# Optimization experiments

Hardware: AMD Instinct MI355X
Metric: run time of the kernel (lower is better)

Reference implementation:

```python
import jax, jax.numpy as jnp
import numpy as np

N, E = 50000, 800000
DIN, DH, H, DOUT = 128, 16, 8, 32  # hidden = H*DH = 128
NEG_SLOPE = 0.2


def setup_inputs() -> dict:
    key = jax.random.key(0)
    ks = jax.random.split(key, 10)
    g = lambda k, shape, fan: jax.random.normal(k, shape, jnp.float32) * (1.0 / np.sqrt(fan))
    return {
        "x": jax.random.normal(ks[0], (N, DIN), jnp.float32),
        "edge_index": jax.random.randint(ks[1], (2, E), 0, N, dtype=jnp.int64),
        # layer 1 (GATv2Conv(DIN, DH, heads=H), concat=True)
        "W1_src": g(ks[2], (DIN, H * DH), DIN),
        "W1_dst": g(ks[3], (DIN, H * DH), DIN),
        "b1_src": jnp.zeros((H * DH,), jnp.float32),
        "b1_dst": jnp.zeros((H * DH,), jnp.float32),
        "att1": g(ks[4], (H, DH), DH),
        "bias1": jnp.zeros((H * DH,), jnp.float32),
        # layer 2 (GATv2Conv(H*DH, DOUT, heads=1))
        "W2_src": g(ks[5], (H * DH, DOUT), H * DH),
        "W2_dst": g(ks[6], (H * DH, DOUT), H * DH),
        "b2_src": jnp.zeros((DOUT,), jnp.float32),
        "b2_dst": jnp.zeros((DOUT,), jnp.float32),
        "att2": g(ks[7], (1, DOUT), DOUT),
        "bias2": jnp.zeros((DOUT,), jnp.float32),
    }


def _gatv2(x, src, dst, Wsrc, Wdst, bsrc, bdst, att, bias):
    # GATv2 conv: e_ij = att . LeakyReLU(Wsrc x_j + Wdst x_i); softmax over j->i; out_i = sum alpha_ij * Wsrc x_j
    n = x.shape[0]
    h, c = att.shape
    xs = (x @ Wsrc + bsrc).reshape(n, h, c)  # source transform (messages)
    xd = (x @ Wdst + bdst).reshape(n, h, c)  # target transform
    msg = xs[src]  # [Etot, h, c]
    e = jax.nn.leaky_relu(msg + xd[dst], NEG_SLOPE)
    logits = jnp.einsum('ehc,hc->eh', e, att)  # [Etot, h]
    m = jax.lax.stop_gradient(jax.ops.segment_max(logits, dst, num_segments=n))
    ex = jnp.exp(logits - m[dst])
    denom = jax.ops.segment_sum(ex, dst, num_segments=n)
    alpha = ex / denom[dst]  # edge softmax per target node, per head
    out = jax.ops.segment_sum(alpha[..., None] * msg, dst, num_segments=n)
    return out.reshape(n, h * c) + bias  # concat=True


def reference(x, edge_index, W1_src, W1_dst, b1_src, b1_dst, att1, bias1,
              W2_src, W2_dst, b2_src, b2_dst, att2, bias2):
    n = x.shape[0]
    loop = jnp.arange(n, dtype=edge_index.dtype)  # add_self_loops=True (PyG default)
    src = jnp.concatenate([edge_index[0], loop])
    dst = jnp.concatenate([edge_index[1], loop])
    h1 = _gatv2(x, src, dst, W1_src, W1_dst, b1_src, b1_dst, att1, bias1)
    h1 = jax.nn.elu(h1)
    h2 = _gatv2(h1, src, dst, W2_src, W2_dst, b2_src, b2_dst, att2, bias2)  # heads=1 -> [N, DOUT]
    return jax.nn.log_softmax(h2, axis=1)
```

## Files before the change

### kernel.cpp

```cpp
#include <hip/hip_runtime.h>
#include <math.h>

#define NEG_SLOPE 0.2f

typedef __attribute__((ext_vector_type(8))) _Float16 h8v;
typedef __attribute__((ext_vector_type(2))) _Float16 h2v;
typedef __attribute__((ext_vector_type(4))) float float4v;

__device__ __forceinline__ h2v u2h(unsigned u) { return __builtin_bit_cast(h2v, u); }
__device__ __forceinline__ unsigned h2u(h2v h) { return __builtin_bit_cast(unsigned, h); }
__device__ __forceinline__ unsigned pk16(float a, float b) {
  h2v r; r.x = (_Float16)a; r.y = (_Float16)b;
  return __builtin_bit_cast(unsigned, r);
}
__device__ __forceinline__ unsigned short f16b(float f) {
  return __builtin_bit_cast(unsigned short, (_Float16)f);
}
__device__ __forceinline__ float fdot2(h2v a, h2v b, float c) {
#if __has_builtin(__builtin_amdgcn_fdot2)
  return __builtin_amdgcn_fdot2(a, b, c, false);
#else
  return fmaf((float)a.x, (float)b.x, fmaf((float)a.y, (float)b.y, c));
#endif
}

__device__ __forceinline__ int block_scan256(int v, int tid, int* ws) {
  const int lane = tid & 63, w = tid >> 6;
  int incl = v;
#pragma unroll
  for (int off = 1; off < 64; off <<= 1) {
    int t = __shfl_up(incl, off);
    if (lane >= off) incl += t;
  }
  if (lane == 63) ws[w] = incl;
  __syncthreads();
  if (tid == 0) {
    int s = 0;
#pragma unroll
    for (int i = 0; i < 4; i++) { int t = ws[i]; ws[4 + i] = s; s += t; }
  }
  __syncthreads();
  return incl - v + ws[4 + w];
}

__global__ __launch_bounds__(256) void pack_all(
    const float* __restrict__ W1s, const float* __restrict__ W1d,
    const float* __restrict__ W2s, const float* __restrict__ W2d,
    unsigned short* __restrict__ B1s, unsigned short* __restrict__ B1d,
    unsigned short* __restrict__ B2s, unsigned short* __restrict__ B2d) {
  int blk = blockIdx.x;
  const float* W; unsigned short* Bp; int C, base;
  if (blk < 8)       { W = W1s; Bp = B1s; C = 128; base = blk; }
  else if (blk < 16) { W = W1d; Bp = B1d; C = 128; base = blk - 8; }
  else if (blk < 18) { W = W2s; Bp = B2s; C = 32;  base = blk - 16; }
  else               { W = W2d; Bp = B2d; C = 32;  base = blk - 18; }
  int idx = base * 256 + threadIdx.x;
  int total = (C / 16) * 4 * 64;
  if (idx >= total) return;
  int lane = idx & 63;
  int kc = (idx >> 6) & 3;
  int t = idx >> 8;
  int n = t * 16 + (lane & 15);
  int k0 = kc * 32 + (lane >> 4) * 8;
  unsigned short* o = Bp + (size_t)idx * 8;
#pragma unroll
  for (int j = 0; j < 8; j++) o[j] = f16b(W[(size_t)(k0 + j) * C + n]);
}

template <int NT, int CVT>
__global__ __launch_bounds__(256) void mfma_xform2(
    const void* __restrict__ Xin,
    const unsigned short* __restrict__ BpS, const unsigned short* __restrict__ BpD,
    const float* __restrict__ bS, const float* __restrict__ bD,
    unsigned int* __restrict__ Ys, unsigned int* __restrict__ Yd, int M) {
  const int wave = threadIdx.x >> 6;
  const int lane = threadIdx.x & 63;
  const int row0 = blockIdx.x * 64 + wave * 16;
  const int m = lane & 15, q = lane >> 4;
  const int arow = min(row0 + m, M - 1);
  h8v a[4];
  if constexpr (CVT) {
    const float* xp = (const float*)Xin + (size_t)arow * 128 + q * 8;
#pragma unroll
    for (int kc = 0; kc < 4; kc++) {
      const float4 f0 = *(const float4*)(xp + kc * 32);
      const float4 f1 = *(const float4*)(xp + kc * 32 + 4);
      uint4 u;
      u.x = pk16(f0.x, f0.y); u.y = pk16(f0.z, f0.w);
      u.z = pk16(f1.x, f1.y); u.w = pk16(f1.z, f1.w);
      a[kc] = __builtin_bit_cast(h8v, u);
    }
  } else {
    const unsigned short* xp = (const unsigned short*)Xin + (size_t)arow * 128 + q * 8;
#pragma unroll
    for (int kc = 0; kc < 4; kc++) a[kc] = *(const h8v*)(xp + kc * 32);
  }
  float4v accS[NT], accD[NT];
#pragma unroll
  for (int t = 0; t < NT; t++) { accS[t] = (float4v)(0.f); accD[t] = (float4v)(0.f); }
#pragma unroll
  for (int kc = 0; kc < 4; kc++) {
#pragma unroll
    for (int t = 0; t < NT; t++) {
      h8v bs = *(const h8v*)(BpS + ((size_t)(t * 4 + kc) * 64 + lane) * 8);
      h8v bd = *(const h8v*)(BpD + ((size_t)(t * 4 + kc) * 64 + lane) * 8);
      accS[t] = __builtin_amdgcn_mfma_f32_16x16x32_f16(a[kc], bs, accS[t], 0, 0, 0);
      accD[t] = __builtin_amdgcn_mfma_f32_16x16x32_f16(a[kc], bd, accD[t], 0, 0, 0);
    }
  }
  const bool even = (m & 1) == 0;
#pragma unroll
  for (int t = 0; t < NT; t++) {
    const int col = t * 16 + m;
    const float bcS = bS[col], bcD = bD[col];
#pragma unroll
    for (int r = 0; r < 4; r++) {
      const int row = row0 + q * 4 + r;
      float vS = accS[t][r] + bcS;
      float vD = accD[t][r] + bcD;
      float pS = __shfl_xor(vS, 1);
      float pD = __shfl_xor(vD, 1);
      if (even && row < M) {
        size_t idx = (size_t)row * (NT * 8) + t * 8 + (m >> 1);
        Ys[idx] = pk16(vS, pS);
        Yd[idx] = pk16(vD, pD);
      }
    }
  }
}

__global__ __launch_bounds__(256) void bucket_hist(
    const int* __restrict__ ei, int* __restrict__ bhist, int N, int E, int NB) {
  __shared__ int cnt[256];
  const int tid = threadIdx.x;
  cnt[tid] = 0;
  __syncthreads();
  const int base = blockIdx.x * 4096;
  const int vn = min(4096, E - base);
#pragma unroll 4
  for (int j = 0; j < 16; j++) {
    int i = j * 256 + tid;
    if (i < vn) {
      int d = ei[E + base + i];
      d = min(max(d, 0), N - 1);
      atomicAdd(&cnt[d >> 8], 1);
    }
  }
  __syncthreads();
  if (tid < NB && cnt[tid]) atomicAdd(&bhist[tid], cnt[tid]);
}

__global__ __launch_bounds__(256) void bucket_scan(
    const int* __restrict__ bhist, int* __restrict__ bbase,
    int* __restrict__ bcur, int NB) {
  __shared__ int ws[8];
  const int tid = threadIdx.x;
  int v = (tid < NB) ? bhist[tid] : 0;
  int excl = block_scan256(v, tid, ws);
  if (tid <= NB) bbase[tid] = excl;
  if (tid < NB) bcur[tid] = excl;
}

__global__ __launch_bounds__(256) void bucket_sort(
    const int* __restrict__ ei, int* __restrict__ bcur,
    unsigned int* __restrict__ pairs, int N, int E, int NB) {
  __shared__ int cnt[256];
  __shared__ int offs[256];
  __shared__ int gbase[256];
  __shared__ int lcur[256];
  __shared__ int ws[8];
  __shared__ unsigned int packed_s[4096];
  __shared__ unsigned char bucket_of[4096];
  const int tid = threadIdx.x;
  cnt[tid] = 0;
  __syncthreads();
  const int base = blockIdx.x * 4096;
  const int vn = min(4096, E - base);
#pragma unroll 4
  for (int j = 0; j < 16; j++) {
    int i = j * 256 + tid;
    if (i < vn) {
      int d = ei[E + base + i];
      d = min(max(d, 0), N - 1);
      atomicAdd(&cnt[d >> 8], 1);
    }
  }
  __syncthreads();
  int excl = block_scan256(cnt[tid], tid, ws);
  offs[tid] = excl;
  lcur[tid] = excl;
  if (tid < NB && cnt[tid]) gbase[tid] = atomicAdd(&bcur[tid], cnt[tid]);
  __syncthreads();
#pragma unroll 4
  for (int j = 0; j < 16; j++) {
    int i = j * 256 + tid;
    if (i < vn) {
      int s = ei[base + i];
      int d = ei[E + base + i];
      s = min(max(s, 0), N - 1);
      d = min(max(d, 0), N - 1);
      int b = d >> 8;
      int slot = atomicAdd(&lcur[b], 1);
      packed_s[slot] = (unsigned)s | ((unsigned)(d & 255) << 16);
      bucket_of[slot] = (unsigned char)b;
    }
  }
  __syncthreads();
  for (int i = tid; i < vn; i += 256) {
    int b = bucket_of[i];
    pairs[gbase[b] + (i - offs[b])] = packed_s[i];
  }
}

__global__ __launch_bounds__(256) void csr_fine(
    const unsigned int* __restrict__ pairs, const int* __restrict__ bbase,
    int* __restrict__ row_ofs, int* __restrict__ src_sorted, int N, int E, int NB) {
  __shared__ int cnt[256];
  __shared__ int cursor[256];
  __shared__ int ws[8];
  const int tid = threadIdx.x;
  const int b = blockIdx.x;
  const int d0 = b << 8;
  const int nd = min(256, N - d0);
  const int pbase = bbase[b];
  const int pcnt = bbase[b + 1] - pbase;
  const int row_base = pbase + d0;
  cnt[tid] = (tid < nd) ? 1 : 0;
  __syncthreads();
  for (int i = tid; i < pcnt; i += 256) {
    unsigned p = pairs[pbase + i];
    atomicAdd(&cnt[(p >> 16) & 255], 1);
  }
  __syncthreads();
  int excl = block_scan256(cnt[tid], tid, ws);
  if (tid < nd) {
    row_ofs[d0 + tid] = row_base + excl;
    src_sorted[row_base + excl] = d0 + tid;
    cursor[tid] = excl + 1;
  }
  if (b == NB - 1 && tid == 0) row_ofs[N] = E + N;
  __syncthreads();
  for (int i = tid; i < pcnt; i += 256) {
    unsigned p = pairs[pbase + i];
    int dl = (p >> 16) & 255;
    int slot = atomicAdd(&cursor[dl], 1);
    src_sorted[row_base + slot] = (int)(p & 0xffffu);
  }
}

__global__ __launch_bounds__(256) void gat1_fused(
    const int* __restrict__ row_ofs, const int* __restrict__ src_sorted,
    const unsigned int* __restrict__ xsb, const unsigned int* __restrict__ xdb,
    const float* __restrict__ att, const float* __restrict__ bias,
    unsigned int* __restrict__ h1b, int N) {
  const int node = (int)((blockIdx.x * 256u + threadIdx.x) >> 6);
  const int lane = threadIdx.x & 63;
  const int l = lane & 15;
  const int g = lane >> 4;
  if (node >= N) return;
  h2v at2[4], xd[4];
  {
    const float4 a01 = *(const float4*)(att + 8 * l);
    const float4 a23 = *(const float4*)(att + 8 * l + 4);
    at2[0] = u2h(pk16(a01.x, a01.y)); at2[1] = u2h(pk16(a01.z, a01.w));
    at2[2] = u2h(pk16(a23.x, a23.y)); at2[3] = u2h(pk16(a23.z, a23.w));
    const uint4 xdp = *(const uint4*)(xdb + (unsigned)(node * 64 + 4 * l));
    xd[0] = u2h(xdp.x); xd[1] = u2h(xdp.y);
    xd[2] = u2h(xdp.z); xd[3] = u2h(xdp.w);
  }
  h2v ns; ns.x = (_Float16)NEG_SLOPE; ns.y = (_Float16)NEG_SLOPE;
  h2v acc[4];
#pragma unroll
  for (int i = 0; i < 4; i++) acc[i] = (h2v)((_Float16)0.f);
  float den = 0.f;
  const int b = row_ofs[node];
  const int cnt = row_ofs[node + 1] - b;
  for (int base = 0; base < cnt; base += 64) {
    const int rem = cnt - base;
    int sidx = (lane < rem) ? src_sorted[b + base + lane] : node;
    const int nIter = min(16, (rem + 3) >> 2);
    int s = __shfl(sidx, g);
    uint4 mp = *(const uint4*)(xsb + (unsigned)(s * 64 + 4 * l));
    for (int it = 0; it < nIter; it++) {
      const uint4 cur = mp;
      const bool v = (base + 4 * it + g) < cnt;
      if (it + 1 < nIter) {
        int sn = __shfl(sidx, 4 * (it + 1) + g);
        mp = *(const uint4*)(xsb + (unsigned)(sn * 64 + 4 * l));
      }
      const h2v m0 = u2h(cur.x), m1 = u2h(cur.y), m2 = u2h(cur.z), m3 = u2h(cur.w);
      h2v t0 = m0 + xd[0]; h2v r0 = __builtin_elementwise_max(t0, t0 * ns);
      h2v t1 = m1 + xd[1]; h2v r1 = __builtin_elementwise_max(t1, t1 * ns);
      h2v t2 = m2 + xd[2]; h2v r2 = __builtin_elementwise_max(t2, t2 * ns);
      h2v t3 = m3 + xd[3]; h2v r3 = __builtin_elementwise_max(t3, t3 * ns);
      float p = fdot2(r0, at2[0], 0.f);
      p = fdot2(r1, at2[1], p);
      p = fdot2(r2, at2[2], p);
      p = fdot2(r3, at2[3], p);
      p += __shfl_xor(p, 1);
      float ex = v ? __expf(p) : 0.f;
      den += ex;
      h2v exh; exh.x = exh.y = (_Float16)ex;
      acc[0] += m0 * exh;
      acc[1] += m1 * exh;
      acc[2] += m2 * exh;
      acc[3] += m3 * exh;
    }
  }
#pragma unroll
  for (int off = 16; off < 64; off <<= 1) {
#pragma unroll
    for (int i = 0; i < 4; i++) acc[i] += u2h(__shfl_xor(h2u(acc[i]), off));
    den += __shfl_xor(den, off);
  }
  if (lane < 16) {
    const float inv = 1.f / den;
    const float4 bc01 = *(const float4*)(bias + 8 * l);
    const float4 bc23 = *(const float4*)(bias + 8 * l + 4);
    float v0 = fmaf((float)acc[0].x, inv, bc01.x);
    float v1 = fmaf((float)acc[0].y, inv, bc01.y);
    float v2 = fmaf((float)acc[1].x, inv, bc01.z);
    float v3 = fmaf((float)acc[1].y, inv, bc01.w);
    float v4 = fmaf((float)acc[2].x, inv, bc23.x);
    float v5 = fmaf((float)acc[2].y, inv, bc23.y);
    float v6 = fmaf((float)acc[3].x, inv, bc23.z);
    float v7 = fmaf((float)acc[3].y, inv, bc23.w);
    v0 = v0 > 0.f ? v0 : __expf(v0) - 1.f;
    v1 = v1 > 0.f ? v1 : __expf(v1) - 1.f;
    v2 = v2 > 0.f ? v2 : __expf(v2) - 1.f;
    v3 = v3 > 0.f ? v3 : __expf(v3) - 1.f;
    v4 = v4 > 0.f ? v4 : __expf(v4) - 1.f;
    v5 = v5 > 0.f ? v5 : __expf(v5) - 1.f;
    v6 = v6 > 0.f ? v6 : __expf(v6) - 1.f;
    v7 = v7 > 0.f ? v7 : __expf(v7) - 1.f;
    uint4 o;
    o.x = pk16(v0, v1); o.y = pk16(v2, v3);
    o.z = pk16(v4, v5); o.w = pk16(v6, v7);
    *(uint4*)(h1b + (unsigned)(node * 64 + 4 * l)) = o;
  }
}

__global__ __launch_bounds__(256) void gat2_fused(
    const int* __restrict__ row_ofs, const int* __restrict__ src_sorted,
    const unsigned int* __restrict__ xsb, const unsigned int* __restrict__ xdb,
    const float* __restrict__ att, const float* __restrict__ bias,
    float* __restrict__ out, int N) {
  const int node = (int)((blockIdx.x * 256u + threadIdx.x) >> 6);
  const int lane = threadIdx.x & 63;
  const int l = lane & 3;
  const int g = lane >> 2;
  if (node >= N) return;
  h2v at2[4], xd[4];
  {
    const float4 a01 = *(const float4*)(att + 8 * l);
    const float4 a23 = *(const float4*)(att + 8 * l + 4);
    at2[0] = u2h(pk16(a01.x, a01.y)); at2[1] = u2h(pk16(a01.z, a01.w));
    at2[2] = u2h(pk16(a23.x, a23.y)); at2[3] = u2h(pk16(a23.z, a23.w));
    const uint4 xdp = *(const uint4*)(xdb + (unsigned)(node * 16 + 4 * l));
    xd[0] = u2h(xdp.x); xd[1] = u2h(xdp.y);
    xd[2] = u2h(xdp.z); xd[3] = u2h(xdp.w);
  }
  h2v ns; ns.x = (_Float16)NEG_SLOPE; ns.y = (_Float16)NEG_SLOPE;
  h2v acc[4];
#pragma unroll
  for (int i = 0; i < 4; i++) acc[i] = (h2v)((_Float16)0.f);
  float den = 0.f;
  const int b = row_ofs[node];
  const int cnt = row_ofs[node + 1] - b;
  for (int base = 0; base < cnt; base += 64) {
    const int rem = cnt - base;
    int sidx = (lane < rem) ? src_sorted[b + base + lane] : node;
    const int nIter = min(4, (rem + 15) >> 4);
    int s = __shfl(sidx, g);
    uint4 mp = *(const uint4*)(xsb + (unsigned)(s * 16 + 4 * l));
    for (int it = 0; it < nIter; it++) {
      const uint4 cur = mp;
      const bool v = (base + 16 * it + g) < cnt;
      if (it + 1 < nIter) {
        int sn = __shfl(sidx, 16 * (it + 1) + g);
        mp = *(const uint4*)(xsb + (unsigned)(sn * 16 + 4 * l));
      }
      const h2v m0 = u2h(cur.x), m1 = u2h(cur.y), m2 = u2h(cur.z), m3 = u2h(cur.w);
      h2v t0 = m0 + xd[0]; h2v r0 = __builtin_elementwise_max(t0, t0 * ns);
      h2v t1 = m1 + xd[1]; h2v r1 = __builtin_elementwise_max(t1, t1 * ns);
      h2v t2 = m2 + xd[2]; h2v r2 = __builtin_elementwise_max(t2, t2 * ns);
      h2v t3 = m3 + xd[3]; h2v r3 = __builtin_elementwise_max(t3, t3 * ns);
      float p = fdot2(r0, at2[0], 0.f);
      p = fdot2(r1, at2[1], p);
      p = fdot2(r2, at2[2], p);
      p = fdot2(r3, at2[3], p);
      p += __shfl_xor(p, 1);
      p += __shfl_xor(p, 2);
      float ex = v ? __expf(p) : 0.f;
      den += ex;
      h2v exh; exh.x = exh.y = (_Float16)ex;
      acc[0] += m0 * exh;
      acc[1] += m1 * exh;
      acc[2] += m2 * exh;
      acc[3] += m3 * exh;
    }
  }
#pragma unroll
  for (int off = 4; off < 64; off <<= 1) {
#pragma unroll
    for (int i = 0; i < 4; i++) acc[i] += u2h(__shfl_xor(h2u(acc[i]), off));
    den += __shfl_xor(den, off);
  }
  if (lane < 4) {
    const float inv = 1.f / den;
    const float4 bc01 = *(const float4*)(bias + 8 * l);
    const float4 bc23 = *(const float4*)(bias + 8 * l + 4);
    float v0 = fmaf((float)acc[0].x, inv, bc01.x);
    float v1 = fmaf((float)acc[0].y, inv, bc01.y);
    float v2 = fmaf((float)acc[1].x, inv, bc01.z);
    float v3 = fmaf((float)acc[1].y, inv, bc01.w);
    float v4 = fmaf((float)acc[2].x, inv, bc23.x);
    float v5 = fmaf((float)acc[2].y, inv, bc23.y);
    float v6 = fmaf((float)acc[3].x, inv, bc23.z);
    float v7 = fmaf((float)acc[3].y, inv, bc23.w);
    float mx = fmaxf(fmaxf(fmaxf(v0, v1), fmaxf(v2, v3)),
                     fmaxf(fmaxf(v4, v5), fmaxf(v6, v7)));
    mx = fmaxf(mx, __shfl_xor(mx, 1));
    mx = fmaxf(mx, __shfl_xor(mx, 2));
    float sum = __expf(v0 - mx) + __expf(v1 - mx) + __expf(v2 - mx) +
                __expf(v3 - mx) + __expf(v4 - mx) + __expf(v5 - mx) +
                __expf(v6 - mx) + __expf(v7 - mx);
    sum += __shfl_xor(sum, 1);
    sum += __shfl_xor(sum, 2);
    const float lse = mx + __logf(sum);
    float* op = out + (size_t)node * 32 + 8 * l;
    *(float4*)op = make_float4(v0 - lse, v1 - lse, v2 - lse, v3 - lse);
    *(float4*)(op + 4) = make_float4(v4 - lse, v5 - lse, v6 - lse, v7 - lse);
  }
}

extern "C" void kernel_launch(void* const* d_in, const int* in_sizes, int n_in,
                              void* d_out, int out_size, void* d_ws, size_t ws_size,
                              hipStream_t stream) {
  const float* x = (const float*)d_in[0];
  const int* ei = (const int*)d_in[1];
  const float* W1s = (const float*)d_in[2];
  const float* W1d = (const float*)d_in[3];
  const float* b1s = (const float*)d_in[4];
  const float* b1d = (const float*)d_in[5];
  const float* att1 = (const float*)d_in[6];
  const float* bias1 = (const float*)d_in[7];
  const float* W2s = (const float*)d_in[8];
  const float* W2d = (const float*)d_in[9];
  const float* b2s = (const float*)d_in[10];
  const float* b2d = (const float*)d_in[11];
  const float* att2 = (const float*)d_in[12];
  const float* bias2 = (const float*)d_in[13];
  float* out = (float*)d_out;

  const int N = in_sizes[0] / 128;
  const int E = in_sizes[1] / 2;
  const int NB = (N + 255) >> 8;

  char* p = (char*)d_ws;
  auto alloc = [&](size_t bytes) { char* r = p; p += (bytes + 63) & ~63ull; return r; };
  unsigned int* xs1b = (unsigned int*)alloc((size_t)N * 64 * 4);
  unsigned int* xd1b = (unsigned int*)alloc((size_t)N * 64 * 4);
  unsigned int* xs2b = (unsigned int*)alloc((size_t)N * 16 * 4);
  unsigned int* xd2b = (unsigned int*)alloc((size_t)N * 16 * 4);
  unsigned int* h1b = (unsigned int*)alloc((size_t)N * 64 * 4);
  unsigned short* Bp1s = (unsigned short*)alloc(8 * 4 * 64 * 8 * 2);
  unsigned short* Bp1d = (unsigned short*)alloc(8 * 4 * 64 * 8 * 2);
  unsigned short* Bp2s = (unsigned short*)alloc(2 * 4 * 64 * 8 * 2);
  unsigned short* Bp2d = (unsigned short*)alloc(2 * 4 * 64 * 8 * 2);
  int* bhist = (int*)alloc((size_t)NB * 4);
  int* bbase = (int*)alloc((size_t)(NB + 1) * 4);
  int* bcur = (int*)alloc((size_t)NB * 4);
  unsigned int* pairs = (unsigned int*)alloc((size_t)E * 4);
  int* row_ofs = (int*)alloc((size_t)(N + 1) * 4);
  int* src_sorted = (int*)alloc((size_t)(E + N) * 4);

  hipMemsetAsync(bhist, 0, (size_t)NB * sizeof(int), stream);

  pack_all<<<20, 256, 0, stream>>>(W1s, W1d, W2s, W2d, Bp1s, Bp1d, Bp2s, Bp2d);

  const int nA = (E + 4095) / 4096;
  bucket_hist<<<nA, 256, 0, stream>>>(ei, bhist, N, E, NB);
  bucket_scan<<<1, 256, 0, stream>>>(bhist, bbase, bcur, NB);
  bucket_sort<<<nA, 256, 0, stream>>>(ei, bcur, pairs, N, E, NB);
  csr_fine<<<NB, 256, 0, stream>>>(pairs, bbase, row_ofs, src_sorted, N, E, NB);

  const int xblocks = (N + 63) / 64;
  mfma_xform2<8, 1><<<xblocks, 256, 0, stream>>>(x, Bp1s, Bp1d, b1s, b1d, xs1b, xd1b, N);

  gat1_fused<<<(N + 3) / 4, 256, 0, stream>>>(row_ofs, src_sorted, xs1b, xd1b,
                                              att1, bias1, h1b, N);

  mfma_xform2<2, 0><<<xblocks, 256, 0, stream>>>(h1b, Bp2s, Bp2d, b2s, b2d,
                                                 xs2b, xd2b, N);

  gat2_fused<<<(N + 3) / 4, 256, 0, stream>>>(row_ofs, src_sorted, xs2b, xd2b,
                                              att2, bias2, out, N);
}
```

Measured before the change: 221.4 us.

## Fuse weight packing into histogram, shrink CSR chunks, double-buffer gather prefetch

```diff
diff --git a/kernel.cpp b/kernel.cpp
--- a/kernel.cpp
+++ b/kernel.cpp
@@ -43,28 +43,150 @@
   return incl - v + ws[4 + w];
 }
 
-__global__ __launch_bounds__(256) void pack_all(
+#define CSR_CHUNK 1024
+
+__global__ __launch_bounds__(256) void pack_hist(
     const float* __restrict__ W1s, const float* __restrict__ W1d,
     const float* __restrict__ W2s, const float* __restrict__ W2d,
     unsigned short* __restrict__ B1s, unsigned short* __restrict__ B1d,
-    unsigned short* __restrict__ B2s, unsigned short* __restrict__ B2d) {
+    unsigned short* __restrict__ B2s, unsigned short* __restrict__ B2d,
+    const int* __restrict__ ei, int* __restrict__ bhist, int N, int E, int NB) {
   int blk = blockIdx.x;
-  const float* W; unsigned short* Bp; int C, base;
-  if (blk < 8)       { W = W1s; Bp = B1s; C = 128; base = blk; }
-  else if (blk < 16) { W = W1d; Bp = B1d; C = 128; base = blk - 8; }
-  else if (blk < 18) { W = W2s; Bp = B2s; C = 32;  base = blk - 16; }
-  else               { W = W2d; Bp = B2d; C = 32;  base = blk - 18; }
-  int idx = base * 256 + threadIdx.x;
-  int total = (C / 16) * 4 * 64;
-  if (idx >= total) return;
-  int lane = idx & 63;
-  int kc = (idx >> 6) & 3;
-  int t = idx >> 8;
-  int n = t * 16 + (lane & 15);
-  int k0 = kc * 32 + (lane >> 4) * 8;
-  unsigned short* o = Bp + (size_t)idx * 8;
-#pragma unroll
-  for (int j = 0; j < 8; j++) o[j] = f16b(W[(size_t)(k0 + j) * C + n]);
+  if (blk < 20) {
+    const float* W; unsigned short* Bp; int C, base;
+    if (blk < 8)       { W = W1s; Bp = B1s; C = 128; base = blk; }
+    else if (blk < 16) { W = W1d; Bp = B1d; C = 128; base = blk - 8; }
+    else if (blk < 18) { W = W2s; Bp = B2s; C = 32;  base = blk - 16; }
+    else               { W = W2d; Bp = B2d; C = 32;  base = blk - 18; }
+    int idx = base * 256 + threadIdx.x;
+    int total = (C / 16) * 4 * 64;
+    if (idx >= total) return;
+    int lane = idx & 63;
+    int kc = (idx >> 6) & 3;
+    int t = idx >> 8;
+    int n = t * 16 + (lane & 15);
+    int k0 = kc * 32 + (lane >> 4) * 8;
+    unsigned short* o = Bp + (size_t)idx * 8;
+#pragma unroll
+    for (int j = 0; j < 8; j++) o[j] = f16b(W[(size_t)(k0 + j) * C + n]);
+    return;
+  }
+  blk -= 20;
+  __shared__ int cnt[256];
+  const int tid = threadIdx.x;
+  cnt[tid] = 0;
+  __syncthreads();
+  const int base = blk * CSR_CHUNK;
+  const int vn = min(CSR_CHUNK, E - base);
+#pragma unroll
+  for (int j = 0; j < CSR_CHUNK / 256; j++) {
+    int i = j * 256 + tid;
+    if (i < vn) {
+      int d = ei[E + base + i];
+      d = min(max(d, 0), N - 1);
+      atomicAdd(&cnt[d >> 8], 1);
+    }
+  }
+  __syncthreads();
+  if (tid < NB && cnt[tid]) atomicAdd(&bhist[tid], cnt[tid]);
+}
+
+__global__ __launch_bounds__(256) void bucket_scan(
+    const int* __restrict__ bhist, int* __restrict__ bbase,
+    int* __restrict__ bcur, int NB) {
+  __shared__ int ws[8];
+  const int tid = threadIdx.x;
+  int v = (tid < NB) ? bhist[tid] : 0;
+  int excl = block_scan256(v, tid, ws);
+  if (tid <= NB) bbase[tid] = excl;
+  if (tid < NB) bcur[tid] = excl;
+}
+
+__global__ __launch_bounds__(256) void bucket_sort(
+    const int* __restrict__ ei, int* __restrict__ bcur,
+    unsigned int* __restrict__ pairs, int N, int E, int NB) {
+  __shared__ int cnt[256];
+  __shared__ int offs[256];
+  __shared__ int gbase[256];
+  __shared__ int lcur[256];
+  __shared__ int ws[8];
+  __shared__ unsigned int packed_s[CSR_CHUNK];
+  __shared__ unsigned char bucket_of[CSR_CHUNK];
+  const int tid = threadIdx.x;
+  cnt[tid] = 0;
+  __syncthreads();
+  const int base = blockIdx.x * CSR_CHUNK;
+  const int vn = min(CSR_CHUNK, E - base);
+#pragma unroll
+  for (int j = 0; j < CSR_CHUNK / 256; j++) {
+    int i = j * 256 + tid;
+    if (i < vn) {
+      int d = ei[E + base + i];
+      d = min(max(d, 0), N - 1);
+      atomicAdd(&cnt[d >> 8], 1);
+    }
+  }
+  __syncthreads();
+  int excl = block_scan256(cnt[tid], tid, ws);
+  offs[tid] = excl;
+  lcur[tid] = excl;
+  if (tid < NB && cnt[tid]) gbase[tid] = atomicAdd(&bcur[tid], cnt[tid]);
+  __syncthreads();
+#pragma unroll
+  for (int j = 0; j < CSR_CHUNK / 256; j++) {
+    int i = j * 256 + tid;
+    if (i < vn) {
+      int s = ei[base + i];
+      int d = ei[E + base + i];
+      s = min(max(s, 0), N - 1);
+      d = min(max(d, 0), N - 1);
+      int b = d >> 8;
+      int slot = atomicAdd(&lcur[b], 1);
+      packed_s[slot] = (unsigned)s | ((unsigned)(d & 255) << 16);
+      bucket_of[slot] = (unsigned char)b;
+    }
+  }
+  __syncthreads();
+  for (int i = tid; i < vn; i += 256) {
+    int b = bucket_of[i];
+    pairs[gbase[b] + (i - offs[b])] = packed_s[i];
+  }
+}
+
+__global__ __launch_bounds__(256) void csr_fine(
+    const unsigned int* __restrict__ pairs, const int* __restrict__ bbase,
+    int* __restrict__ row_ofs, int* __restrict__ src_sorted, int N, int E, int NB) {
+  __shared__ int cnt[256];
+  __shared__ int cursor[256];
+  __shared__ int ws[8];
+  const int tid = threadIdx.x;
+  const int b = blockIdx.x;
+  const int d0 = b << 8;
+  const int nd = min(256, N - d0);
+  const int pbase = bbase[b];
+  const int pcnt = bbase[b + 1] - pbase;
+  const int row_base = pbase + d0;
+  cnt[tid] = (tid < nd) ? 1 : 0;
+  __syncthreads();
+  for (int i = tid; i < pcnt; i += 256) {
+    unsigned p = pairs[pbase + i];
+    atomicAdd(&cnt[(p >> 16) & 255], 1);
+  }
+  __syncthreads();
+  int excl = block_scan256(cnt[tid], tid, ws);
+  if (tid < nd) {
+    row_ofs[d0 + tid] = row_base + excl;
+    src_sorted[row_base + excl] = d0 + tid;
+    cursor[tid] = excl + 1;
+  }
+  if (b == NB - 1 && tid == 0) row_ofs[N] = E + N;
+  __syncthreads();
+  for (int i = tid; i < pcnt; i += 256) {
+    unsigned p = pairs[pbase + i];
+    int dl = (p >> 16) & 255;
+    int slot = atomicAdd(&cursor[dl], 1);
+    src_sorted[row_base + slot] = (int)(p & 0xffffu);
+  }
 }
 
 template <int NT, int CVT>
@@ -126,125 +248,6 @@
         Yd[idx] = pk16(vD, pD);
       }
     }
-  }
-}
-
-__global__ __launch_bounds__(256) void bucket_hist(
-    const int* __restrict__ ei, int* __restrict__ bhist, int N, int E, int NB) {
-  __shared__ int cnt[256];
-  const int tid = threadIdx.x;
-  cnt[tid] = 0;
-  __syncthreads();
-  const int base = blockIdx.x * 4096;
-  const int vn = min(4096, E - base);
-#pragma unroll 4
-  for (int j = 0; j < 16; j++) {
-    int i = j * 256 + tid;
-    if (i < vn) {
-      int d = ei[E + base + i];
-      d = min(max(d, 0), N - 1);
-      atomicAdd(&cnt[d >> 8], 1);
-    }
-  }
-  __syncthreads();
-  if (tid < NB && cnt[tid]) atomicAdd(&bhist[tid], cnt[tid]);
-}
-
-__global__ __launch_bounds__(256) void bucket_scan(
-    const int* __restrict__ bhist, int* __restrict__ bbase,
-    int* __restrict__ bcur, int NB) {
-  __shared__ int ws[8];
-  const int tid = threadIdx.x;
-  int v = (tid < NB) ? bhist[tid] : 0;
-  int excl = block_scan256(v, tid, ws);
-  if (tid <= NB) bbase[tid] = excl;
-  if (tid < NB) bcur[tid] = excl;
-}
-
-__global__ __launch_bounds__(256) void bucket_sort(
-    const int* __restrict__ ei, int* __restrict__ bcur,
-    unsigned int* __restrict__ pairs, int N, int E, int NB) {
-  __shared__ int cnt[256];
-  __shared__ int offs[256];
-  __shared__ int gbase[256];
-  __shared__ int lcur[256];
-  __shared__ int ws[8];
-  __shared__ unsigned int packed_s[4096];
-  __shared__ unsigned char bucket_of[4096];
-  const int tid = threadIdx.x;
-  cnt[tid] = 0;
-  __syncthreads();
-  const int base = blockIdx.x * 4096;
-  const int vn = min(4096, E - base);
-#pragma unroll 4
-  for (int j = 0; j < 16; j++) {
-    int i = j * 256 + tid;
-    if (i < vn) {
-      int d = ei[E + base + i];
-      d = min(max(d, 0), N - 1);
-      atomicAdd(&cnt[d >> 8], 1);
-    }
-  }
-  __syncthreads();
-  int excl = block_scan256(cnt[tid], tid, ws);
-  offs[tid] = excl;
-  lcur[tid] = excl;
-  if (tid < NB && cnt[tid]) gbase[tid] = atomicAdd(&bcur[tid], cnt[tid]);
-  __syncthreads();
-#pragma unroll 4
-  for (int j = 0; j < 16; j++) {
-    int i = j * 256 + tid;
-    if (i < vn) {
-      int s = ei[base + i];
-      int d = ei[E + base + i];
-      s = min(max(s, 0), N - 1);
-      d = min(max(d, 0), N - 1);
-      int b = d >> 8;
-      int slot = atomicAdd(&lcur[b], 1);
-      packed_s[slot] = (unsigned)s | ((unsigned)(d & 255) << 16);
-      bucket_of[slot] = (unsigned char)b;
-    }
-  }
-  __syncthreads();
-  for (int i = tid; i < vn; i += 256) {
-    int b = bucket_of[i];
-    pairs[gbase[b] + (i - offs[b])] = packed_s[i];
-  }
-}
-
-__global__ __launch_bounds__(256) void csr_fine(
-    const unsigned int* __restrict__ pairs, const int* __restrict__ bbase,
-    int* __restrict__ row_ofs, int* __restrict__ src_sorted, int N, int E, int NB) {
-  __shared__ int cnt[256];
-  __shared__ int cursor[256];
-  __shared__ int ws[8];
-  const int tid = threadIdx.x;
-  const int b = blockIdx.x;
-  const int d0 = b << 8;
-  const int nd = min(256, N - d0);
-  const int pbase = bbase[b];
-  const int pcnt = bbase[b + 1] - pbase;
-  const int row_base = pbase + d0;
-  cnt[tid] = (tid < nd) ? 1 : 0;
-  __syncthreads();
-  for (int i = tid; i < pcnt; i += 256) {
-    unsigned p = pairs[pbase + i];
-    atomicAdd(&cnt[(p >> 16) & 255], 1);
-  }
-  __syncthreads();
-  int excl = block_scan256(cnt[tid], tid, ws);
-  if (tid < nd) {
-    row_ofs[d0 + tid] = row_base + excl;
-    src_sorted[row_base + excl] = d0 + tid;
-    cursor[tid] = excl + 1;
-  }
-  if (b == NB - 1 && tid == 0) row_ofs[N] = E + N;
-  __syncthreads();
-  for (int i = tid; i < pcnt; i += 256) {
-    unsigned p = pairs[pbase + i];
-    int dl = (p >> 16) & 255;
-    int slot = atomicAdd(&cursor[dl], 1);
-    src_sorted[row_base + slot] = (int)(p & 0xffffu);
   }
 }
 
@@ -275,37 +278,51 @@
   float den = 0.f;
   const int b = row_ofs[node];
   const int cnt = row_ofs[node + 1] - b;
+
+  auto process = [&](const uint4 cur, bool valid) {
+    const h2v m0 = u2h(cur.x), m1 = u2h(cur.y), m2 = u2h(cur.z), m3 = u2h(cur.w);
+    h2v t0 = m0 + xd[0]; h2v r0 = __builtin_elementwise_max(t0, t0 * ns);
+    h2v t1 = m1 + xd[1]; h2v r1 = __builtin_elementwise_max(t1, t1 * ns);
+    h2v t2 = m2 + xd[2]; h2v r2 = __builtin_elementwise_max(t2, t2 * ns);
+    h2v t3 = m3 + xd[3]; h2v r3 = __builtin_elementwise_max(t3, t3 * ns);
+    float p = fdot2(r0, at2[0], 0.f);
+    p = fdot2(r1, at2[1], p);
+    p = fdot2(r2, at2[2], p);
+    p = fdot2(r3, at2[3], p);
+    p += __shfl_xor(p, 1);
+    float ex = valid ? __expf(p) : 0.f;
+    den += ex;
+    h2v exh; exh.x = exh.y = (_Float16)ex;
+    acc[0] += m0 * exh;
+    acc[1] += m1 * exh;
+    acc[2] += m2 * exh;
+    acc[3] += m3 * exh;
+  };
+
   for (int base = 0; base < cnt; base += 64) {
     const int rem = cnt - base;
-    int sidx = (lane < rem) ? src_sorted[b + base + lane] : node;
-    const int nIter = min(16, (rem + 3) >> 2);
-    int s = __shfl(sidx, g);
-    uint4 mp = *(const uint4*)(xsb + (unsigned)(s * 64 + 4 * l));
-    for (int it = 0; it < nIter; it++) {
-      const uint4 cur = mp;
-      const bool v = (base + 4 * it + g) < cnt;
-      if (it + 1 < nIter) {
-        int sn = __shfl(sidx, 4 * (it + 1) + g);
-        mp = *(const uint4*)(xsb + (unsigned)(sn * 64 + 4 * l));
+    const int ne = min(64, rem);
+    int sidx = (lane < ne) ? src_sorted[b + base + lane] : node;
+    const int nIter = (ne + 3) >> 2;
+    const int nFull = ne >> 2;
+    const int tailc = ne & 3;
+    int s0 = __shfl(sidx, g);
+    uint4 mpA = *(const uint4*)(xsb + (unsigned)(s0 * 64 + 4 * l));
+    uint4 mpB;
+    if (nIter > 1) {
+      int s1 = __shfl(sidx, 4 + g);
+      mpB = *(const uint4*)(xsb + (unsigned)(s1 * 64 + 4 * l));
+    }
+    for (int it = 0; it < nFull; it++) {
+      const uint4 cur = mpA;
+      mpA = mpB;
+      if (it + 2 < nIter) {
+        int sn = __shfl(sidx, 4 * (it + 2) + g);
+        mpB = *(const uint4*)(xsb + (unsigned)(sn * 64 + 4 * l));
       }
-      const h2v m0 = u2h(cur.x), m1 = u2h(cur.y), m2 = u2h(cur.z), m3 = u2h(cur.w);
-      h2v t0 = m0 + xd[0]; h2v r0 = __builtin_elementwise_max(t0, t0 * ns);
-      h2v t1 = m1 + xd[1]; h2v r1 = __builtin_elementwise_max(t1, t1 * ns);
-      h2v t2 = m2 + xd[2]; h2v r2 = __builtin_elementwise_max(t2, t2 * ns);
-      h2v t3 = m3 + xd[3]; h2v r3 = __builtin_elementwise_max(t3, t3 * ns);
-      float p = fdot2(r0, at2[0], 0.f);
-      p = fdot2(r1, at2[1], p);
-      p = fdot2(r2, at2[2], p);
-      p = fdot2(r3, at2[3], p);
-      p += __shfl_xor(p, 1);
-      float ex = v ? __expf(p) : 0.f;
-      den += ex;
-      h2v exh; exh.x = exh.y = (_Float16)ex;
-      acc[0] += m0 * exh;
-      acc[1] += m1 * exh;
-      acc[2] += m2 * exh;
-      acc[3] += m3 * exh;
-    }
+      process(cur, true);
+    }
+    if (tailc) process(mpA, g < tailc);
   }
 #pragma unroll
   for (int off = 16; off < 64; off <<= 1) {
@@ -367,38 +384,52 @@
   float den = 0.f;
   const int b = row_ofs[node];
   const int cnt = row_ofs[node + 1] - b;
+
+  auto process = [&](const uint4 cur, bool valid) {
+    const h2v m0 = u2h(cur.x), m1 = u2h(cur.y), m2 = u2h(cur.z), m3 = u2h(cur.w);
+    h2v t0 = m0 + xd[0]; h2v r0 = __builtin_elementwise_max(t0, t0 * ns);
+    h2v t1 = m1 + xd[1]; h2v r1 = __builtin_elementwise_max(t1, t1 * ns);
+    h2v t2 = m2 + xd[2]; h2v r2 = __builtin_elementwise_max(t2, t2 * ns);
+    h2v t3 = m3 + xd[3]; h2v r3 = __builtin_elementwise_max(t3, t3 * ns);
+    float p = fdot2(r0, at2[0], 0.f);
+    p = fdot2(r1, at2[1], p);
+    p = fdot2(r2, at2[2], p);
+    p = fdot2(r3, at2[3], p);
+    p += __shfl_xor(p, 1);
+    p += __shfl_xor(p, 2);
+    float ex = valid ? __expf(p) : 0.f;
+    den += ex;
+    h2v exh; exh.x = exh.y = (_Float16)ex;
+    acc[0] += m0 * exh;
+    acc[1] += m1 * exh;
+    acc[2] += m2 * exh;
+    acc[3] += m3 * exh;
+  };
+
   for (int base = 0; base < cnt; base += 64) {
     const int rem = cnt - base;
-    int sidx = (lane < rem) ? src_sorted[b + base + lane] : node;
-    const int nIter = min(4, (rem + 15) >> 4);
-    int s = __shfl(sidx, g);
-    uint4 mp = *(const uint4*)(xsb + (unsigned)(s * 16 + 4 * l));
-    for (int it = 0; it < nIter; it++) {
-      const uint4 cur = mp;
-      const bool v = (base + 16 * it + g) < cnt;
-      if (it + 1 < nIter) {
-        int sn = __shfl(sidx, 16 * (it + 1) + g);
-        mp = *(const uint4*)(xsb + (unsigned)(sn * 16 + 4 * l));
+    const int ne = min(64, rem);
+    int sidx = (lane < ne) ? src_sorted[b + base + lane] : node;
+    const int nIter = (ne + 15) >> 4;
+    const int nFull = ne >> 4;
+    const int tailc = ne & 15;
+    int s0 = __shfl(sidx, g);
+    uint4 mpA = *(const uint4*)(xsb + (unsigned)(s0 * 16 + 4 * l));
+    uint4 mpB;
+    if (nIter > 1) {
+      int s1 = __shfl(sidx, 16 + g);
+      mpB = *(const uint4*)(xsb + (unsigned)(s1 * 16 + 4 * l));
+    }
+    for (int it = 0; it < nFull; it++) {
+      const uint4 cur = mpA;
+      mpA = mpB;
+      if (it + 2 < nIter) {
+        int sn = __shfl(sidx, 16 * (it + 2) + g);
+        mpB = *(const uint4*)(xsb + (unsigned)(sn * 16 + 4 * l));
       }
-      const h2v m0 = u2h(cur.x), m1 = u2h(cur.y), m2 = u2h(cur.z), m3 = u2h(cur.w);
-      h2v t0 = m0 + xd[0]; h2v r0 = __builtin_elementwise_max(t0, t0 * ns);
-      h2v t1 = m1 + xd[1]; h2v r1 = __builtin_elementwise_max(t1, t1 * ns);
-      h2v t2 = m2 + xd[2]; h2v r2 = __builtin_elementwise_max(t2, t2 * ns);
-      h2v t3 = m3 + xd[3]; h2v r3 = __builtin_elementwise_max(t3, t3 * ns);
-      float p = fdot2(r0, at2[0], 0.f);
-      p = fdot2(r1, at2[1], p);
-      p = fdot2(r2, at2[2], p);
-      p = fdot2(r3, at2[3], p);
-      p += __shfl_xor(p, 1);
-      p += __shfl_xor(p, 2);
-      float ex = v ? __expf(p) : 0.f;
-      den += ex;
-      h2v exh; exh.x = exh.y = (_Float16)ex;
-      acc[0] += m0 * exh;
-      acc[1] += m1 * exh;
-      acc[2] += m2 * exh;
-      acc[3] += m3 * exh;
-    }
+      process(cur, true);
+    }
+    if (tailc) process(mpA, g < tailc);
   }
 #pragma unroll
   for (int off = 4; off < 64; off <<= 1) {
@@ -477,10 +508,9 @@
 
   hipMemsetAsync(bhist, 0, (size_t)NB * sizeof(int), stream);
 
-  pack_all<<<20, 256, 0, stream>>>(W1s, W1d, W2s, W2d, Bp1s, Bp1d, Bp2s, Bp2d);
-
-  const int nA = (E + 4095) / 4096;
-  bucket_hist<<<nA, 256, 0, stream>>>(ei, bhist, N, E, NB);
+  const int nA = (E + CSR_CHUNK - 1) / CSR_CHUNK;
+  pack_hist<<<20 + nA, 256, 0, stream>>>(W1s, W1d, W2s, W2d, Bp1s, Bp1d, Bp2s, Bp2d,
+                                         ei, bhist, N, E, NB);
   bucket_scan<<<1, 256, 0, stream>>>(bhist, bbase, bcur, NB);
   bucket_sort<<<nA, 256, 0, stream>>>(ei, bcur, pairs, N, E, NB);
   csr_fine<<<NB, 256, 0, stream>>>(pairs, bbase, row_ofs, src_sorted, N, E, NB);
```

After: 231.5 us. 1.05x slower.
